# Kernel optimization log

Hardware: AMD Instinct MI355X
Metric: run time of the kernel (lower is better)

## Reference

```python
import jax, jax.numpy as jnp
import numpy as np

H = 8  # num_heads

def setup_inputs() -> dict:
    key = jax.random.key(0)
    ks = jax.random.split(key, 10)
    B, N, C = 2048, 50, 256
    x = jax.random.normal(ks[0], (B, N, C), dtype=jnp.float32)
    adj = jax.random.uniform(ks[1], (B, N, N), dtype=jnp.float32)
    matrix = jax.random.normal(ks[2], (B, N, N), dtype=jnp.float32)
    s = 0.02
    Wq = jax.random.normal(ks[3], (C, C), dtype=jnp.float32) * s
    bq = jnp.zeros((C,), dtype=jnp.float32)
    Wk = jax.random.normal(ks[4], (C, C), dtype=jnp.float32) * s
    bk = jnp.zeros((C,), dtype=jnp.float32)
    Wa = jax.random.normal(ks[5], (N * H, N), dtype=jnp.float32) * s
    ba = jnp.zeros((N * H,), dtype=jnp.float32)
    Wm = jax.random.normal(ks[6], (N * H, N), dtype=jnp.float32) * s
    bm = jnp.zeros((N * H,), dtype=jnp.float32)
    lambdas = jnp.tile(jnp.array([[1.0, 0.0, 0.0]], dtype=jnp.float32), (H, 1))
    return {"x": x, "adj": adj, "matrix": matrix, "Wq": Wq, "bq": bq,
            "Wk": Wk, "bk": bk, "Wa": Wa, "ba": ba, "Wm": Wm, "bm": bm,
            "lambdas": lambdas}

def reference(x, adj, matrix, Wq, bq, Wk, bk, Wa, ba, Wm, bm, lambdas):
    B, N, C = x.shape
    D = C // H
    # torch Linear: y = x @ W.T + b
    q = (jnp.einsum('bnc,dc->bnd', x, Wq) + bq).reshape(B, N, H, D).transpose(0, 2, 1, 3)
    k = (jnp.einsum('bnc,dc->bnd', x, Wk) + bk).reshape(B, N, H, D).transpose(0, 2, 1, 3)
    # NOTE: original code computes v with self.k (faithful to source)
    v = k
    # scale uses full dim C (x.shape[-1]), not head_dim, as in source
    attn = jax.nn.softmax(jnp.einsum('bhnd,bhmd->bhnm', q, k) * (C ** -0.5), axis=-1)
    adj_a = jax.nn.softmax(
        (jnp.einsum('bnm,km->bnk', adj, Wa) + ba).reshape(B, N, H, N).transpose(0, 2, 1, 3), axis=-1)
    mat_a = jax.nn.softmax(
        (jnp.einsum('bnm,km->bnk', matrix, Wm) + bm).reshape(B, N, H, N).transpose(0, 2, 1, 3), axis=-1)
    lam = jax.nn.softmax(lambdas, axis=-1)  # [H, 3]
    l0 = lam[:, 0][None, :, None, None]
    l1 = lam[:, 1][None, :, None, None]
    l2 = lam[:, 2][None, :, None, None]
    mix = l0 * attn + l1 * adj_a + l2 * mat_a  # [B, H, N, N]
    out = jnp.einsum('bhnm,bhmd->bhnd', mix, v).transpose(0, 2, 1, 3).reshape(B, N, C)
    return out
```

## Files before the change

kernel.cpp:

```cpp
#include <hip/hip_runtime.h>
#include <stdint.h>


typedef __attribute__((ext_vector_type(8))) short short8;
typedef __attribute__((ext_vector_type(4))) float f32x4;
typedef __attribute__((ext_vector_type(2))) unsigned u32x2;
typedef __attribute__((ext_vector_type(4))) unsigned u32x4;
typedef unsigned short u16;

#define L2E 1.4426950408889634f

__device__ __forceinline__ u16 f2bf(float f) {
  unsigned int u = __float_as_uint(f);
  u = (u + 0x7FFFu + ((u >> 16) & 1u)) >> 16;
  return (u16)u;
}
__device__ __forceinline__ unsigned cvt_pk_bf16(float a, float b) {
  unsigned r;
  asm("v_cvt_pk_bf16_f32 %0, %1, %2" : "=v"(r) : "v"(a), "v"(b));
  return r;
}
__device__ __forceinline__ float exp2_fast(float x) {
#if __has_builtin(__builtin_amdgcn_exp2f)
  return __builtin_amdgcn_exp2f(x);
#else
  return __expf(x * 0.6931471805599453f);
#endif
}

__global__ __launch_bounds__(256) void cast_all(
    const float* __restrict__ adj, const float* __restrict__ mat,
    const float* __restrict__ Wq, const float* __restrict__ Wk,
    const float* __restrict__ Wa, const float* __restrict__ Wm,
    const float* __restrict__ ba, const float* __restrict__ bm,
    u16* __restrict__ da, u16* __restrict__ dm, u16* __restrict__ wqk,
    u16* __restrict__ wab, u16* __restrict__ wmb,
    float* __restrict__ bap, float* __restrict__ bmp, float* __restrict__ maskv,
    u16* __restrict__ qws, u16* __restrict__ kws) {
  const int blk = blockIdx.x, tid = threadIdx.x;
  if (blk < 2048) {
    const int total8 = (102416 * 64) / 8;
    for (int i8 = blk * 256 + tid; i8 < total8; i8 += 2048 * 256) {
      int r = i8 >> 3, c = (i8 & 7) * 8;
      short8 oa = (short8){0,0,0,0,0,0,0,0};
      short8 om = (short8){0,0,0,0,0,0,0,0};
      if (r < 102400) {
        size_t base = (size_t)r * 50;
#pragma unroll
        for (int p = 0; p < 4; ++p) {
          int col = c + 2 * p;
          if (col < 50) {
            float2 va = *(const float2*)(adj + base + col);
            float2 vm = *(const float2*)(mat + base + col);
            oa[2*p] = f2bf(va.x); oa[2*p+1] = f2bf(va.y);
            om[2*p] = f2bf(vm.x); om[2*p+1] = f2bf(vm.y);
          }
        }
      }
      *(short8*)(da + (size_t)i8 * 8) = oa;
      *(short8*)(dm + (size_t)i8 * 8) = om;
    }
  } else if (blk < 2112) {
    int idx8 = (blk - 2048) * 256 + tid;
    int r = idx8 >> 5, c = (idx8 & 31) * 8;
    const float* src = (r < 256) ? (Wq + (size_t)r * 256 + c)
                                 : (Wk + (size_t)(r - 256) * 256 + c);
    float4 v0 = *(const float4*)(src);
    float4 v1 = *(const float4*)(src + 4);
    short8 o;
    o[0] = f2bf(v0.x); o[1] = f2bf(v0.y); o[2] = f2bf(v0.z); o[3] = f2bf(v0.w);
    o[4] = f2bf(v1.x); o[5] = f2bf(v1.y); o[6] = f2bf(v1.z); o[7] = f2bf(v1.w);
    *(short8*)(wqk + (size_t)idx8 * 8) = o;
  } else if (blk < 2216) {
    int idx = (blk - 2112) * 256 + tid;
    int r = idx >> 6, c = idx & 63;
    float va = 0.f, vm = 0.f;
    if (r < 400 && c < 50) { va = Wa[r * 50 + c]; vm = Wm[r * 50 + c]; }
    wab[idx] = f2bf(va); wmb[idx] = f2bf(vm);
  } else {
    short8 z = (short8){0,0,0,0,0,0,0,0};
    *(short8*)(qws + (size_t)819200 * 32 + tid * 8) = z;
    *(short8*)(kws + (size_t)819200 * 32 + tid * 8) = z;
#pragma unroll
    for (int j = 0; j < 2; ++j) {
      int idx = tid + 256 * j;
      int hh = idx >> 6, m = idx & 63;
      bap[idx] = (m < 50) ? ba[hh * 50 + m] * L2E : -1.0e30f;
      bmp[idx] = (m < 50) ? bm[hh * 50 + m] * L2E : -1.0e30f;
    }
    if (tid < 64) maskv[tid] = (tid < 50) ? 0.f : -1.0e30f;
  }
}

__global__ __launch_bounds__(256) void proj_kernel(
    const float* __restrict__ x, const u16* __restrict__ wqk,
    const float* __restrict__ bq, const float* __restrict__ bk,
    u16* __restrict__ qws, u16* __restrict__ kws) {
  __shared__ char xa[64 * 512];
  __shared__ char wb[64 * 512];
  const int tid = threadIdx.x;
  const int m0 = blockIdx.x * 64;

#pragma unroll
  for (int t = 0; t < 16; ++t) {
    int idx = tid + t * 256;
    int r = idx >> 6, c4 = idx & 63;
    float4 v = *(const float4*)(x + (size_t)(m0 + r) * 256 + c4 * 4);
    unsigned long long pk = (unsigned long long)f2bf(v.x)
                          | ((unsigned long long)f2bf(v.y) << 16)
                          | ((unsigned long long)f2bf(v.z) << 32)
                          | ((unsigned long long)f2bf(v.w) << 48);
    int byte = (r * 512 + c4 * 8) ^ ((r & 7) << 4);
    *(unsigned long long*)(xa + byte) = pk;
  }
  __syncthreads();

  const int w = tid >> 6, l = tid & 63, lo = l & 15, g = l >> 4;
  short8 a[8];
  const int ra = 16 * w + lo;
#pragma unroll
  for (int ks = 0; ks < 8; ++ks)
    a[ks] = *(const short8*)(xa + ((ra * 512 + ks * 64 + g * 16) ^ ((ra & 7) << 4)));
  size_t mb[4];
#pragma unroll
  for (int i = 0; i < 4; ++i) {
    int m = m0 + 16 * w + 4 * g + i;
    int b = m / 50;
    int n = m - 50 * b;
    mb[i] = (size_t)b * 12800 + (size_t)n * 32;
  }

  for (int nt = 0; nt < 8; ++nt) {
    __syncthreads();
#pragma unroll
    for (int t = 0; t < 8; ++t) {
      int idx = tid + t * 256;
      int r = idx >> 5, c8 = idx & 31;
      short8 v = *(const short8*)(wqk + (size_t)(nt * 64 + r) * 256 + c8 * 8);
      int byte = (r * 512 + c8 * 16) ^ ((r & 7) << 4);
      *(short8*)(wb + byte) = v;
    }
    __syncthreads();

    f32x4 acc[4];
#pragma unroll
    for (int tj = 0; tj < 4; ++tj) acc[tj] = (f32x4){0.f, 0.f, 0.f, 0.f};
#pragma unroll
    for (int ks = 0; ks < 8; ++ks) {
#pragma unroll
      for (int tj = 0; tj < 4; ++tj) {
        int rb = 16 * tj + lo;
        short8 bb = *(const short8*)(wb + ((rb * 512 + ks * 64 + g * 16) ^ ((rb & 7) << 4)));
        acc[tj] = __builtin_amdgcn_mfma_f32_16x16x32_bf16(a[ks], bb, acc[tj], 0, 0, 0);
      }
    }
    const int n0 = nt * 64;
#pragma unroll
    for (int tj = 0; tj < 4; ++tj) {
      int j = n0 + 16 * tj + lo;
      int jj = j & 255;
      float bias = (j < 256) ? bq[jj] : bk[jj];
      u16* dst = (j < 256) ? qws : kws;
      int hh = jj >> 5, d = jj & 31;
#pragma unroll
      for (int i = 0; i < 4; ++i)
        dst[mb[i] + (size_t)hh * 1600 + d] = f2bf(acc[tj][i] + bias);
    }
  }
}

__device__ __forceinline__ void sm_store(
    f32x4 (&S)[4], const f32x4 (&bml)[4], float sl2e, float lam,
    u16* pb, int buf, int lo, int g) {
  float p[4][4];
#pragma unroll
  for (int ti = 0; ti < 4; ++ti)
#pragma unroll
    for (int i = 0; i < 4; ++i)
      p[ti][i] = exp2_fast(S[ti][i] * sl2e + bml[ti][i]);
  float t0 = (p[0][0] + p[0][1]) + (p[0][2] + p[0][3]);
  float t1 = (p[1][0] + p[1][1]) + (p[1][2] + p[1][3]);
  float t2 = (p[2][0] + p[2][1]) + (p[2][2] + p[2][3]);
  float t3 = (p[3][0] + p[3][1]) + (p[3][2] + p[3][3]);
  float sum = (t0 + t1) + (t2 + t3);
  sum += __shfl_xor(sum, 16);
  sum += __shfl_xor(sum, 32);
  float r = lam * __builtin_amdgcn_rcpf(sum);
#pragma unroll
  for (int ti = 0; ti < 4; ++ti) {
    u32x2 pk;
    pk.x = cvt_pk_bf16(p[ti][0] * r, p[ti][1] * r);
    pk.y = cvt_pk_bf16(p[ti][2] * r, p[ti][3] * r);
    *(volatile u32x2*)(pb + buf * 1152 + lo * 72 + 16 * ti + 4 * g) = pk;
  }
}

__device__ __forceinline__ void pv_acc(
    const u16* pb, int buf, const short8 (&vbS)[2][2], f32x4 (&Otj)[2],
    int lo, int g) {
#pragma unroll
  for (int ks = 0; ks < 2; ++ks) {
    u32x4 t = *(const volatile u32x4*)(pb + buf * 1152 + lo * 72 + ks * 32 + g * 8);
    short8 pa = __builtin_bit_cast(short8, t);
#pragma unroll
    for (int tjv = 0; tjv < 2; ++tjv)
      Otj[tjv] = __builtin_amdgcn_mfma_f32_16x16x32_bf16(pa, vbS[tjv][ks], Otj[tjv], 0, 0, 0);
  }
}

__global__ __launch_bounds__(256) void attn_kernel(
    const u16* __restrict__ qws, const u16* __restrict__ kws,
    const u16* __restrict__ adjb, const u16* __restrict__ matb,
    const u16* __restrict__ wab, const u16* __restrict__ wmb,
    const float* __restrict__ bap, const float* __restrict__ bmp,
    const float* __restrict__ maskv,
    const float* __restrict__ lambdas, float* __restrict__ out) {
  __shared__ u16 smem[4][2304];
  const int tid = threadIdx.x;
  const int w = tid >> 6, l = tid & 63, lo = l & 15, g = l >> 4;
  const int bh = blockIdx.x * 4 + w;
  const int b = bh >> 3, h = bh & 7;
  u16* sh = smem[w];

  const u16* kbase = kws + (size_t)bh * 1600;
  const u16* qbase = qws + (size_t)bh * 1600;

  short8 kr[4];
#pragma unroll
  for (int ch = 0; ch < 4; ++ch)
    kr[ch] = *(const short8*)(kbase + (size_t)l * 32 + ch * 8);
  short8 af1[4], qf1[4];
#pragma unroll
  for (int ti = 0; ti < 4; ++ti)
    af1[ti] = *(const short8*)(kbase + (size_t)(lo + 16 * ti) * 32 + g * 8);
#pragma unroll
  for (int tj = 0; tj < 4; ++tj)
    qf1[tj] = *(const short8*)(qbase + (size_t)(lo + 16 * tj) * 32 + g * 8);
  const u16* bB2 = adjb + (size_t)b * 3200;
  short8 bf2[4][2];
#pragma unroll
  for (int tj = 0; tj < 4; ++tj)
#pragma unroll
    for (int ks = 0; ks < 2; ++ks)
      bf2[tj][ks] = *(const short8*)(bB2 + (size_t)(lo + 16 * tj) * 64 + ks * 32 + g * 8);
  __builtin_amdgcn_sched_barrier(0);

  float la = lambdas[h * 3 + 0], lb = lambdas[h * 3 + 1], lc = lambdas[h * 3 + 2];
  float lmx = fmaxf(la, fmaxf(lb, lc));
  float e0 = __expf(la - lmx), e1 = __expf(lb - lmx), e2 = __expf(lc - lmx);
  float einv = 1.f / (e0 + e1 + e2);
  float lam0 = e0 * einv, lam1 = e1 * einv, lam2 = e2 * einv;

#pragma unroll
  for (int ch = 0; ch < 4; ++ch)
#pragma unroll
    for (int jj = 0; jj < 8; ++jj)
      *(volatile u16*)(sh + (ch * 8 + jj) * 72 + l) = (u16)kr[ch][jj];
  short8 vb[2][2];
#pragma unroll
  for (int tjv = 0; tjv < 2; ++tjv)
#pragma unroll
    for (int ks = 0; ks < 2; ++ks) {
      u32x4 t = *(const volatile u32x4*)(sh + (lo + 16 * tjv) * 72 + ks * 32 + g * 8);
      vb[tjv][ks] = __builtin_bit_cast(short8, t);
    }

  f32x4 O[4][2];
#pragma unroll
  for (int tj = 0; tj < 4; ++tj)
#pragma unroll
    for (int tjv = 0; tjv < 2; ++tjv) O[tj][tjv] = (f32x4){0.f, 0.f, 0.f, 0.f};

  {
    f32x4 bml[4];
#pragma unroll
    for (int ti = 0; ti < 4; ++ti)
      bml[ti] = *(const f32x4*)(maskv + 16 * ti + 4 * g);
#pragma unroll
    for (int tj = 0; tj < 4; ++tj) {
      f32x4 S[4];
#pragma unroll
      for (int ti = 0; ti < 4; ++ti) S[ti] = (f32x4){0.f, 0.f, 0.f, 0.f};
#pragma unroll
      for (int ti = 0; ti < 4; ++ti)
        S[ti] = __builtin_amdgcn_mfma_f32_16x16x32_bf16(af1[ti], qf1[tj], S[ti], 0, 0, 0);
      sm_store(S, bml, 0.0625f * L2E, lam0, sh, tj & 1, lo, g);
      pv_acc(sh, tj & 1, vb, O[tj], lo, g);
    }
  }

  const u16* bB3 = matb + (size_t)b * 3200;
  short8 bf3[4][2];
#pragma unroll
  for (int tj = 0; tj < 4; ++tj)
#pragma unroll
    for (int ks = 0; ks < 2; ++ks)
      bf3[tj][ks] = *(const short8*)(bB3 + (size_t)(lo + 16 * tj) * 64 + ks * 32 + g * 8);
  __builtin_amdgcn_sched_barrier(0);

  {
    const u16* aBase = wab + (size_t)h * 3200;
    short8 afw[4][2];
#pragma unroll
    for (int ti = 0; ti < 4; ++ti)
#pragma unroll
      for (int ks = 0; ks < 2; ++ks)
        afw[ti][ks] = *(const short8*)(aBase + (size_t)(lo + 16 * ti) * 64 + ks * 32 + g * 8);
    f32x4 bml[4];
#pragma unroll
    for (int ti = 0; ti < 4; ++ti)
      bml[ti] = *(const f32x4*)(bap + h * 64 + 16 * ti + 4 * g);
#pragma unroll
    for (int tj = 0; tj < 4; ++tj) {
      f32x4 S[4];
#pragma unroll
      for (int ti = 0; ti < 4; ++ti) S[ti] = (f32x4){0.f, 0.f, 0.f, 0.f};
#pragma unroll
      for (int ti = 0; ti < 4; ++ti)
        S[ti] = __builtin_amdgcn_mfma_f32_16x16x32_bf16(afw[ti][0], bf2[tj][0], S[ti], 0, 0, 0);
#pragma unroll
      for (int ti = 0; ti < 4; ++ti)
        S[ti] = __builtin_amdgcn_mfma_f32_16x16x32_bf16(afw[ti][1], bf2[tj][1], S[ti], 0, 0, 0);
      sm_store(S, bml, L2E, lam1, sh, tj & 1, lo, g);
      pv_acc(sh, tj & 1, vb, O[tj], lo, g);
    }
  }
  {
    const u16* aBase = wmb + (size_t)h * 3200;
    short8 afw[4][2];
#pragma unroll
    for (int ti = 0; ti < 4; ++ti)
#pragma unroll
      for (int ks = 0; ks < 2; ++ks)
        afw[ti][ks] = *(const short8*)(aBase + (size_t)(lo + 16 * ti) * 64 + ks * 32 + g * 8);
    f32x4 bml[4];
#pragma unroll
    for (int ti = 0; ti < 4; ++ti)
      bml[ti] = *(const f32x4*)(bmp + h * 64 + 16 * ti + 4 * g);
#pragma unroll
    for (int tj = 0; tj < 4; ++tj) {
      f32x4 S[4];
#pragma unroll
      for (int ti = 0; ti < 4; ++ti) S[ti] = (f32x4){0.f, 0.f, 0.f, 0.f};
#pragma unroll
      for (int ti = 0; ti < 4; ++ti)
        S[ti] = __builtin_amdgcn_mfma_f32_16x16x32_bf16(afw[ti][0], bf3[tj][0], S[ti], 0, 0, 0);
#pragma unroll
      for (int ti = 0; ti < 4; ++ti)
        S[ti] = __builtin_amdgcn_mfma_f32_16x16x32_bf16(afw[ti][1], bf3[tj][1], S[ti], 0, 0, 0);
      sm_store(S, bml, L2E, lam2, sh, tj & 1, lo, g);
      pv_acc(sh, tj & 1, vb, O[tj], lo, g);
    }
  }

  float* ob = out + (size_t)b * 12800 + h * 32;
#pragma unroll
  for (int tj = 0; tj < 4; ++tj)
#pragma unroll
    for (int i = 0; i < 4; ++i) {
      int n = 16 * tj + 4 * g + i;
      if (n < 50) {
#pragma unroll
        for (int tjv = 0; tjv < 2; ++tjv)
          ob[(size_t)n * 256 + 16 * tjv + lo] = O[tj][tjv][i];
      }
    }
}

extern "C" void kernel_launch(void* const* d_in, const int* in_sizes, int n_in,
                              void* d_out, int out_size, void* d_ws, size_t ws_size,
                              hipStream_t stream) {
  const float* x       = (const float*)d_in[0];
  const float* adj     = (const float*)d_in[1];
  const float* mat     = (const float*)d_in[2];
  const float* Wq      = (const float*)d_in[3];
  const float* bq      = (const float*)d_in[4];
  const float* Wk      = (const float*)d_in[5];
  const float* bk      = (const float*)d_in[6];
  const float* Wa      = (const float*)d_in[7];
  const float* ba      = (const float*)d_in[8];
  const float* Wm      = (const float*)d_in[9];
  const float* bm      = (const float*)d_in[10];
  const float* lambdas = (const float*)d_in[11];
  float* out = (float*)d_out;

  char* ws = (char*)d_ws;
  u16* wqk    = (u16*)ws; ws += (size_t)512 * 256 * 2;
  u16* wab    = (u16*)ws; ws += (size_t)416 * 64 * 2;
  u16* wmb    = (u16*)ws; ws += (size_t)416 * 64 * 2;
  float* bap  = (float*)ws; ws += (size_t)512 * 4;
  float* bmp  = (float*)ws; ws += (size_t)512 * 4;
  float* mskv = (float*)ws; ws += (size_t)64 * 4;
  u16* adjb   = (u16*)ws; ws += (size_t)102416 * 64 * 2;
  u16* matb   = (u16*)ws; ws += (size_t)102416 * 64 * 2;
  u16* qws    = (u16*)ws; ws += (size_t)819264 * 32 * 2;
  u16* kws    = (u16*)ws; ws += (size_t)819264 * 32 * 2;

  cast_all<<<2217, 256, 0, stream>>>(adj, mat, Wq, Wk, Wa, Wm, ba, bm,
                                     adjb, matb, wqk, wab, wmb,
                                     bap, bmp, mskv, qws, kws);
  proj_kernel<<<1600, 256, 0, stream>>>(x, wqk, bq, bk, qws, kws);
  attn_kernel<<<4096, 256, 0, stream>>>(qws, kws, adjb, matb, wab, wmb,
                                        bap, bmp, mskv, lambdas, out);
}
```

Measured before the change: 232.4 us.

## Fuse adj/matrix bf16 cast into attention kernel and add MFMA priority hints

Drops the separate pass that converts adj and matrix to padded bf16 in workspace. The attention kernel now reads the fp32 rows directly and converts each B-fragment in registers, clamping padded rows and zeroing padded columns. This removes a full write-then-read round trip of two large tensors. It also loads Q/K fragments lazily per tile instead of up front, merges the two adj/mat phases into one loop, and wraps the MFMA sections in s_setprio. The catch is that each batch's fp32 adj and matrix rows are now read by all 8 head blocks, using unaligned float2 loads.

```diff
diff --git a/kernel.cpp b/kernel.cpp
--- a/kernel.cpp
+++ b/kernel.cpp
@@ -28,40 +28,16 @@
 #endif
 }
 
-__global__ __launch_bounds__(256) void cast_all(
-    const float* __restrict__ adj, const float* __restrict__ mat,
+__global__ __launch_bounds__(256) void cast_small(
     const float* __restrict__ Wq, const float* __restrict__ Wk,
     const float* __restrict__ Wa, const float* __restrict__ Wm,
     const float* __restrict__ ba, const float* __restrict__ bm,
-    u16* __restrict__ da, u16* __restrict__ dm, u16* __restrict__ wqk,
-    u16* __restrict__ wab, u16* __restrict__ wmb,
+    u16* __restrict__ wqk, u16* __restrict__ wab, u16* __restrict__ wmb,
     float* __restrict__ bap, float* __restrict__ bmp, float* __restrict__ maskv,
     u16* __restrict__ qws, u16* __restrict__ kws) {
   const int blk = blockIdx.x, tid = threadIdx.x;
-  if (blk < 2048) {
-    const int total8 = (102416 * 64) / 8;
-    for (int i8 = blk * 256 + tid; i8 < total8; i8 += 2048 * 256) {
-      int r = i8 >> 3, c = (i8 & 7) * 8;
-      short8 oa = (short8){0,0,0,0,0,0,0,0};
-      short8 om = (short8){0,0,0,0,0,0,0,0};
-      if (r < 102400) {
-        size_t base = (size_t)r * 50;
-#pragma unroll
-        for (int p = 0; p < 4; ++p) {
-          int col = c + 2 * p;
-          if (col < 50) {
-            float2 va = *(const float2*)(adj + base + col);
-            float2 vm = *(const float2*)(mat + base + col);
-            oa[2*p] = f2bf(va.x); oa[2*p+1] = f2bf(va.y);
-            om[2*p] = f2bf(vm.x); om[2*p+1] = f2bf(vm.y);
-          }
-        }
-      }
-      *(short8*)(da + (size_t)i8 * 8) = oa;
-      *(short8*)(dm + (size_t)i8 * 8) = om;
-    }
-  } else if (blk < 2112) {
-    int idx8 = (blk - 2048) * 256 + tid;
+  if (blk < 64) {
+    int idx8 = blk * 256 + tid;
     int r = idx8 >> 5, c = (idx8 & 31) * 8;
     const float* src = (r < 256) ? (Wq + (size_t)r * 256 + c)
                                  : (Wk + (size_t)(r - 256) * 256 + c);
@@ -71,8 +47,8 @@
     o[0] = f2bf(v0.x); o[1] = f2bf(v0.y); o[2] = f2bf(v0.z); o[3] = f2bf(v0.w);
     o[4] = f2bf(v1.x); o[5] = f2bf(v1.y); o[6] = f2bf(v1.z); o[7] = f2bf(v1.w);
     *(short8*)(wqk + (size_t)idx8 * 8) = o;
-  } else if (blk < 2216) {
-    int idx = (blk - 2112) * 256 + tid;
+  } else if (blk < 168) {
+    int idx = (blk - 64) * 256 + tid;
     int r = idx >> 6, c = idx & 63;
     float va = 0.f, vm = 0.f;
     if (r < 400 && c < 50) { va = Wa[r * 50 + c]; vm = Wm[r * 50 + c]; }
@@ -169,6 +145,25 @@
   }
 }
 
+__device__ __forceinline__ short8 f32frag(const float* __restrict__ row, int g, int ks) {
+  short8 r = (short8){0,0,0,0,0,0,0,0};
+  const int m0 = ks * 32 + g * 8;
+  if (m0 <= 40) {
+    u32x4 wv;
+#pragma unroll
+    for (int p = 0; p < 4; ++p) {
+      float2 v = *(const float2*)(row + m0 + 2 * p);
+      wv[p] = cvt_pk_bf16(v.x, v.y);
+    }
+    r = __builtin_bit_cast(short8, wv);
+  } else if (m0 == 48) {
+    float2 v = *(const float2*)(row + 48);
+    u32x4 wv = (u32x4){cvt_pk_bf16(v.x, v.y), 0u, 0u, 0u};
+    r = __builtin_bit_cast(short8, wv);
+  }
+  return r;
+}
+
 __device__ __forceinline__ void sm_store(
     f32x4 (&S)[4], const f32x4 (&bml)[4], float sl2e, float lam,
     u16* pb, int buf, int lo, int g) {
@@ -198,6 +193,7 @@
 __device__ __forceinline__ void pv_acc(
     const u16* pb, int buf, const short8 (&vbS)[2][2], f32x4 (&Otj)[2],
     int lo, int g) {
+  __builtin_amdgcn_s_setprio(1);
 #pragma unroll
   for (int ks = 0; ks < 2; ++ks) {
     u32x4 t = *(const volatile u32x4*)(pb + buf * 1152 + lo * 72 + ks * 32 + g * 8);
@@ -206,11 +202,12 @@
     for (int tjv = 0; tjv < 2; ++tjv)
       Otj[tjv] = __builtin_amdgcn_mfma_f32_16x16x32_bf16(pa, vbS[tjv][ks], Otj[tjv], 0, 0, 0);
   }
+  __builtin_amdgcn_s_setprio(0);
 }
 
 __global__ __launch_bounds__(256) void attn_kernel(
     const u16* __restrict__ qws, const u16* __restrict__ kws,
-    const u16* __restrict__ adjb, const u16* __restrict__ matb,
+    const float* __restrict__ adjf, const float* __restrict__ matf,
     const u16* __restrict__ wab, const u16* __restrict__ wmb,
     const float* __restrict__ bap, const float* __restrict__ bmp,
     const float* __restrict__ maskv,
@@ -222,40 +219,22 @@
   const int b = bh >> 3, h = bh & 7;
   u16* sh = smem[w];
 
-  const u16* kbase = kws + (size_t)bh * 1600;
-  const u16* qbase = qws + (size_t)bh * 1600;
-
-  short8 kr[4];
-#pragma unroll
-  for (int ch = 0; ch < 4; ++ch)
-    kr[ch] = *(const short8*)(kbase + (size_t)l * 32 + ch * 8);
-  short8 af1[4], qf1[4];
-#pragma unroll
-  for (int ti = 0; ti < 4; ++ti)
-    af1[ti] = *(const short8*)(kbase + (size_t)(lo + 16 * ti) * 32 + g * 8);
-#pragma unroll
-  for (int tj = 0; tj < 4; ++tj)
-    qf1[tj] = *(const short8*)(qbase + (size_t)(lo + 16 * tj) * 32 + g * 8);
-  const u16* bB2 = adjb + (size_t)b * 3200;
-  short8 bf2[4][2];
-#pragma unroll
-  for (int tj = 0; tj < 4; ++tj)
-#pragma unroll
-    for (int ks = 0; ks < 2; ++ks)
-      bf2[tj][ks] = *(const short8*)(bB2 + (size_t)(lo + 16 * tj) * 64 + ks * 32 + g * 8);
-  __builtin_amdgcn_sched_barrier(0);
-
   float la = lambdas[h * 3 + 0], lb = lambdas[h * 3 + 1], lc = lambdas[h * 3 + 2];
   float lmx = fmaxf(la, fmaxf(lb, lc));
   float e0 = __expf(la - lmx), e1 = __expf(lb - lmx), e2 = __expf(lc - lmx);
   float einv = 1.f / (e0 + e1 + e2);
   float lam0 = e0 * einv, lam1 = e1 * einv, lam2 = e2 * einv;
 
-#pragma unroll
-  for (int ch = 0; ch < 4; ++ch)
-#pragma unroll
-    for (int jj = 0; jj < 8; ++jj)
-      *(volatile u16*)(sh + (ch * 8 + jj) * 72 + l) = (u16)kr[ch][jj];
+  {
+    const u16* kr = kws + (size_t)bh * 1600 + (size_t)l * 32;
+#pragma unroll
+    for (int ch = 0; ch < 4; ++ch) {
+      short8 v = *(const short8*)(kr + ch * 8);
+#pragma unroll
+      for (int jj = 0; jj < 8; ++jj)
+        *(volatile u16*)(sh + (ch * 8 + jj) * 72 + l) = (u16)v[jj];
+    }
+  }
   short8 vb[2][2];
 #pragma unroll
   for (int tjv = 0; tjv < 2; ++tjv)
@@ -272,34 +251,37 @@
     for (int tjv = 0; tjv < 2; ++tjv) O[tj][tjv] = (f32x4){0.f, 0.f, 0.f, 0.f};
 
   {
+    short8 af[4];
+#pragma unroll
+    for (int ti = 0; ti < 4; ++ti)
+      af[ti] = *(const short8*)(kws + (size_t)bh * 1600 + (size_t)(lo + 16 * ti) * 32 + g * 8);
     f32x4 bml[4];
 #pragma unroll
     for (int ti = 0; ti < 4; ++ti)
       bml[ti] = *(const f32x4*)(maskv + 16 * ti + 4 * g);
 #pragma unroll
     for (int tj = 0; tj < 4; ++tj) {
+      short8 qf = *(const short8*)(qws + (size_t)bh * 1600 + (size_t)(lo + 16 * tj) * 32 + g * 8);
       f32x4 S[4];
 #pragma unroll
       for (int ti = 0; ti < 4; ++ti) S[ti] = (f32x4){0.f, 0.f, 0.f, 0.f};
+      __builtin_amdgcn_s_setprio(1);
 #pragma unroll
       for (int ti = 0; ti < 4; ++ti)
-        S[ti] = __builtin_amdgcn_mfma_f32_16x16x32_bf16(af1[ti], qf1[tj], S[ti], 0, 0, 0);
+        S[ti] = __builtin_amdgcn_mfma_f32_16x16x32_bf16(af[ti], qf, S[ti], 0, 0, 0);
+      __builtin_amdgcn_s_setprio(0);
       sm_store(S, bml, 0.0625f * L2E, lam0, sh, tj & 1, lo, g);
       pv_acc(sh, tj & 1, vb, O[tj], lo, g);
     }
   }
 
-  const u16* bB3 = matb + (size_t)b * 3200;
-  short8 bf3[4][2];
-#pragma unroll
-  for (int tj = 0; tj < 4; ++tj)
-#pragma unroll
-    for (int ks = 0; ks < 2; ++ks)
-      bf3[tj][ks] = *(const short8*)(bB3 + (size_t)(lo + 16 * tj) * 64 + ks * 32 + g * 8);
-  __builtin_amdgcn_sched_barrier(0);
-
-  {
-    const u16* aBase = wab + (size_t)h * 3200;
+#pragma unroll
+  for (int ph = 0; ph < 2; ++ph) {
+    const u16* aBase = (ph == 0 ? wab : wmb) + (size_t)h * 3200;
+    const float* bRow = (ph == 0 ? adjf : matf) + (size_t)b * 2500;
+    const float* bPad = (ph == 0 ? bap : bmp) + h * 64;
+    float lamp = (ph == 0) ? lam1 : lam2;
+
     short8 afw[4][2];
 #pragma unroll
     for (int ti = 0; ti < 4; ++ti)
@@ -309,46 +291,26 @@
     f32x4 bml[4];
 #pragma unroll
     for (int ti = 0; ti < 4; ++ti)
-      bml[ti] = *(const f32x4*)(bap + h * 64 + 16 * ti + 4 * g);
+      bml[ti] = *(const f32x4*)(bPad + 16 * ti + 4 * g);
+
 #pragma unroll
     for (int tj = 0; tj < 4; ++tj) {
+      int n = lo + 16 * tj;
+      const float* row = bRow + (size_t)(n < 50 ? n : 49) * 50;
+      short8 bf0 = f32frag(row, g, 0);
+      short8 bf1 = f32frag(row, g, 1);
       f32x4 S[4];
 #pragma unroll
       for (int ti = 0; ti < 4; ++ti) S[ti] = (f32x4){0.f, 0.f, 0.f, 0.f};
+      __builtin_amdgcn_s_setprio(1);
 #pragma unroll
       for (int ti = 0; ti < 4; ++ti)
-        S[ti] = __builtin_amdgcn_mfma_f32_16x16x32_bf16(afw[ti][0], bf2[tj][0], S[ti], 0, 0, 0);
+        S[ti] = __builtin_amdgcn_mfma_f32_16x16x32_bf16(afw[ti][0], bf0, S[ti], 0, 0, 0);
 #pragma unroll
       for (int ti = 0; ti < 4; ++ti)
-        S[ti] = __builtin_amdgcn_mfma_f32_16x16x32_bf16(afw[ti][1], bf2[tj][1], S[ti], 0, 0, 0);
-      sm_store(S, bml, L2E, lam1, sh, tj & 1, lo, g);
-      pv_acc(sh, tj & 1, vb, O[tj], lo, g);
-    }
-  }
-  {
-    const u16* aBase = wmb + (size_t)h * 3200;
-    short8 afw[4][2];
-#pragma unroll
-    for (int ti = 0; ti < 4; ++ti)
-#pragma unroll
-      for (int ks = 0; ks < 2; ++ks)
-        afw[ti][ks] = *(const short8*)(aBase + (size_t)(lo + 16 * ti) * 64 + ks * 32 + g * 8);
-    f32x4 bml[4];
-#pragma unroll
-    for (int ti = 0; ti < 4; ++ti)
-      bml[ti] = *(const f32x4*)(bmp + h * 64 + 16 * ti + 4 * g);
-#pragma unroll
-    for (int tj = 0; tj < 4; ++tj) {
-      f32x4 S[4];
-#pragma unroll
-      for (int ti = 0; ti < 4; ++ti) S[ti] = (f32x4){0.f, 0.f, 0.f, 0.f};
-#pragma unroll
-      for (int ti = 0; ti < 4; ++ti)
-        S[ti] = __builtin_amdgcn_mfma_f32_16x16x32_bf16(afw[ti][0], bf3[tj][0], S[ti], 0, 0, 0);
-#pragma unroll
-      for (int ti = 0; ti < 4; ++ti)
-        S[ti] = __builtin_amdgcn_mfma_f32_16x16x32_bf16(afw[ti][1], bf3[tj][1], S[ti], 0, 0, 0);
-      sm_store(S, bml, L2E, lam2, sh, tj & 1, lo, g);
+        S[ti] = __builtin_amdgcn_mfma_f32_16x16x32_bf16(afw[ti][1], bf1, S[ti], 0, 0, 0);
+      __builtin_amdgcn_s_setprio(0);
+      sm_store(S, bml, L2E, lamp, sh, tj & 1, lo, g);
       pv_acc(sh, tj & 1, vb, O[tj], lo, g);
     }
   }
@@ -391,15 +353,12 @@
   float* bap  = (float*)ws; ws += (size_t)512 * 4;
   float* bmp  = (float*)ws; ws += (size_t)512 * 4;
   float* mskv = (float*)ws; ws += (size_t)64 * 4;
-  u16* adjb   = (u16*)ws; ws += (size_t)102416 * 64 * 2;
-  u16* matb   = (u16*)ws; ws += (size_t)102416 * 64 * 2;
   u16* qws    = (u16*)ws; ws += (size_t)819264 * 32 * 2;
   u16* kws    = (u16*)ws; ws += (size_t)819264 * 32 * 2;
 
-  cast_all<<<2217, 256, 0, stream>>>(adj, mat, Wq, Wk, Wa, Wm, ba, bm,
-                                     adjb, matb, wqk, wab, wmb,
-                                     bap, bmp, mskv, qws, kws);
+  cast_small<<<169, 256, 0, stream>>>(Wq, Wk, Wa, Wm, ba, bm,
+                                      wqk, wab, wmb, bap, bmp, mskv, qws, kws);
   proj_kernel<<<1600, 256, 0, stream>>>(x, wqk, bq, bk, qws, kws);
-  attn_kernel<<<4096, 256, 0, stream>>>(qws, kws, adjb, matb, wab, wmb,
+  attn_kernel<<<4096, 256, 0, stream>>>(qws, kws, adj, mat, wab, wmb,
                                         bap, bmp, mskv, lambdas, out);
 }
```

After: 262.0 us. 1.13x slower.
